# Kernel tuning notes

Hardware: AMD Instinct MI355X
Metric: run time of the kernel (lower is better)

The kernel has to match this reference:

```python
import jax, jax.numpy as jnp
import numpy as np

B, L, DM = 16, 1024, 512
DI, ST, DC, RK, OD = 1024, 16, 4, 32, 128


def setup_inputs() -> dict:
    key = jax.random.key(0)
    ks = jax.random.split(key, 10)
    s = 0.02
    x = jax.random.normal(ks[0], (B, L, DM), dtype=jnp.float32)
    W_in = jax.random.normal(ks[1], (DM, 2 * DI), dtype=jnp.float32) * s
    conv_w = jax.random.normal(ks[2], (DI, DC), dtype=jnp.float32) * 0.2
    conv_b = jax.random.normal(ks[3], (DI,), dtype=jnp.float32) * s
    W_xproj = jax.random.normal(ks[4], (DI, RK + 2 * ST), dtype=jnp.float32) * s
    W_dt = jax.random.normal(ks[5], (RK, DI), dtype=jnp.float32) * s
    b_dt = jax.random.normal(ks[6], (DI,), dtype=jnp.float32) * s
    # S4D-real init: A_log[d, n] = log(n+1)
    A_log = jnp.log(jnp.tile(jnp.arange(1, ST + 1, dtype=jnp.float32)[None, :], (DI, 1)))
    Dp = jnp.ones((DI,), dtype=jnp.float32)
    W_out = jax.random.normal(ks[7], (DI, DM), dtype=jnp.float32) * s
    W_fc = jax.random.normal(ks[8], (L * DM, OD), dtype=jnp.float32) * 0.002
    b_fc = jnp.zeros((OD,), dtype=jnp.float32)
    return {"x": x, "W_in": W_in, "conv_w": conv_w, "conv_b": conv_b,
            "W_xproj": W_xproj, "W_dt": W_dt, "b_dt": b_dt, "A_log": A_log,
            "Dp": Dp, "W_out": W_out, "W_fc": W_fc, "b_fc": b_fc}


def _silu(v):
    return v * jax.nn.sigmoid(v)


def reference(x, W_in, conv_w, conv_b, W_xproj, W_dt, b_dt, A_log, Dp, W_out, W_fc, b_fc):
    b, l, dm = x.shape
    di, dc = conv_w.shape
    rk = W_dt.shape[0]
    st = A_log.shape[1]
    # in_proj -> split into x branch and gate z
    xz = x @ W_in                                # [B,L,2*DI]
    xin, z = jnp.split(xz, 2, axis=-1)
    # causal depthwise conv1d, kernel size dc, truncated to length l
    xp = jnp.pad(xin, ((0, 0), (dc - 1, 0), (0, 0)))
    conv = conv_b
    for j in range(dc):                          # fixed small kernel loop
        conv = conv + xp[:, j:j + l, :] * conv_w[:, j]
    xc = _silu(conv)                             # [B,L,DI]
    # input-dependent dt, B, C
    x_dbl = xc @ W_xproj                         # [B,L,RK+2*ST]
    dt = jax.nn.softplus(x_dbl[..., :rk] @ W_dt + b_dt)   # [B,L,DI]
    Bm = x_dbl[..., rk:rk + st]                  # [B,L,ST]
    Cm = x_dbl[..., rk + st:]                    # [B,L,ST]
    A = -jnp.exp(A_log)                          # [DI,ST]
    # selective scan: h_t = exp(dt_t*A)*h_{t-1} + dt_t*B_t*u_t ; y_t = C_t . h_t
    def step(h, inp):
        dt_t, B_t, C_t, u_t = inp                # [B,DI],[B,ST],[B,ST],[B,DI]
        dA = jnp.exp(dt_t[:, :, None] * A)       # [B,DI,ST]
        h = h * dA + (dt_t * u_t)[:, :, None] * B_t[:, None, :]
        y = jnp.einsum('bds,bs->bd', h, C_t)
        return h, y
    h0 = jnp.zeros((b, di, st), dtype=x.dtype)
    seq = (dt.transpose(1, 0, 2), Bm.transpose(1, 0, 2),
           Cm.transpose(1, 0, 2), xc.transpose(1, 0, 2))
    _, ys = jax.lax.scan(step, h0, seq)          # ys: [L,B,DI]
    y = ys.transpose(1, 0, 2) + Dp * xc          # skip connection
    y = y * _silu(z)                             # gate
    out = y @ W_out                              # [B,L,DM]
    # flatten + fc
    return out.reshape(b, -1) @ W_fc + b_fc      # [B,OD]
```

## Files before the change

### kernel.cpp

```cpp
#include <hip/hip_runtime.h>
#include <hip/hip_bf16.h>

typedef __hip_bfloat16 bf16;
typedef __bf16 bf8v __attribute__((ext_vector_type(8)));
typedef __bf16 bf4v __attribute__((ext_vector_type(4)));
typedef float f4v __attribute__((ext_vector_type(4)));

static __device__ __forceinline__ float tf(const bf16 v) { return __bfloat162float(v); }

static __device__ __forceinline__ float ldv(const void* p, size_t i, bool f32) {
    return f32 ? ((const float*)p)[i] : tf(((const bf16*)p)[i]);
}

static __device__ __forceinline__ void gld_lds16(const bf16* g, __bf16* l) {
    __builtin_amdgcn_global_load_lds(
        (const __attribute__((address_space(1))) void*)g,
        (__attribute__((address_space(3))) void*)l, 16, 0, 0);
}

constexpr int Bz = 16, Lz = 1024, DM = 512, DI = 1024, ST = 16, DC = 4, RK = 32, OD = 128;
constexpr int Mrows = Bz * Lz;
constexpr int XD = RK + 2 * ST;
constexpr int NC = 16, CT = Lz / NC;
constexpr int FC_KC = 512;
constexpr int FC_BLOCKS = (Lz * DM) / FC_KC;

__global__ void detect_kernel(const void* __restrict__ xp, int* __restrict__ flag) {
    int i = blockIdx.x * 256 + threadIdx.x;
    const bf16* p = (const bf16*)xp;
    float v = tf(p[(size_t)i * 64]);
    if (!(fabsf(v) < 1e4f)) atomicAdd(flag, 1);
}

__global__ __launch_bounds__(256) void canon_kernel(const void* __restrict__ src,
                                                    bf16* __restrict__ dst,
                                                    const int* __restrict__ flag) {
    const bool f = (*flag != 0);
    size_t base = ((size_t)blockIdx.x * 256 + threadIdx.x) * 8;
    if (!f) {
        *(uint4*)((__bf16*)dst + base) = *(const uint4*)((const bf16*)src + base);
    } else {
        f4v a = *(const f4v*)((const float*)src + base);
        f4v b = *(const f4v*)((const float*)src + base + 4);
        bf8v o;
        #pragma unroll
        for (int j = 0; j < 4; ++j) { o[j] = (__bf16)a[j]; o[j + 4] = (__bf16)b[j]; }
        *(bf8v*)((__bf16*)dst + base) = o;
    }
}

__global__ __launch_bounds__(256) void transpose3_kernel(const void* __restrict__ W0,
                                                         const void* __restrict__ W1,
                                                         const void* __restrict__ W2,
                                                         bf16* __restrict__ T0,
                                                         bf16* __restrict__ T1,
                                                         bf16* __restrict__ T2,
                                                         const int* __restrict__ flag) {
    const bool f = (*flag != 0);
    __shared__ float tile[32][33];
    int bid = blockIdx.x;
    const void* W; bf16* Wt; int K, N, n0, k0;
    if (bid < 1024) {
        W = W0; Wt = T0; K = DM; N = 2 * DI; n0 = (bid & 63) * 32; k0 = (bid >> 6) * 32;
    } else if (bid < 1536) {
        int b = bid - 1024;
        W = W1; Wt = T1; K = DI; N = DM; n0 = (b & 15) * 32; k0 = (b >> 4) * 32;
    } else {
        int b = bid - 1536;
        W = W2; Wt = T2; K = DI; N = XD; n0 = (b & 1) * 32; k0 = (b >> 1) * 32;
    }
    int c = threadIdx.x & 31, r4 = threadIdx.x >> 5;
    #pragma unroll
    for (int i = 0; i < 4; ++i) {
        int r = r4 + i * 8;
        tile[r][c] = ldv(W, (size_t)(k0 + r) * N + n0 + c, f);
    }
    __syncthreads();
    #pragma unroll
    for (int i = 0; i < 4; ++i) {
        int rr = r4 + i * 8;
        Wt[(size_t)(n0 + rr) * K + k0 + c] = __float2bfloat16(tile[c][rr]);
    }
}

template <int NT, bool SPLIT, bool CF32, int GXL>
__global__ __launch_bounds__(256) void gemm_bt(const bf16* __restrict__ A, int lda,
                                               const bf16* __restrict__ Bt, int ldb,
                                               void* __restrict__ C0, void* __restrict__ C1,
                                               int ldc, int K) {
    constexpr int MI = (NT == 128) ? 4 : 2;
    constexpr int NI = 4;
    constexpr int GX = 1 << GXL;
    __shared__ __align__(16) __bf16 As[2][128 * 32];
    __shared__ __align__(16) __bf16 Bs[2][NT * 32];
    const int tid = threadIdx.x, lane = tid & 63, w = tid >> 6;
    const int l15 = lane & 15, quad = lane >> 4;
    const int wm = (NT == 128) ? (w >> 1) * 64 : w * 32;
    const int wn = (NT == 128) ? (w & 1) * 64 : 0;

    const int nwg = GX * gridDim.y;
    const int bid = blockIdx.y * GX + blockIdx.x;
    const int swz = (bid & 7) * (nwg >> 3) + (bid >> 3);
    const int m0 = (swz >> GXL) * 128, n0 = (swz & (GX - 1)) * NT;

    f4v acc[MI][NI];
    #pragma unroll
    for (int i = 0; i < MI; ++i)
        #pragma unroll
        for (int j = 0; j < NI; ++j)
            #pragma unroll
            for (int r = 0; r < 4; ++r) acc[i][j][r] = 0.f;

    const int arow = w * 32 + (lane >> 2), ach = lane & 3;
    const int brow = w * 16 + (lane >> 2);

    auto stage = [&](int bi, int k0) {
        {
            const bf16* g0 = A + (size_t)(m0 + arow) * lda + k0 + ach * 8;
            gld_lds16(g0, &As[bi][w * 1024 + lane * 8]);
            gld_lds16(g0 + (size_t)16 * lda, &As[bi][w * 1024 + 512 + lane * 8]);
        }
        if constexpr (NT == 128) {
            const bf16* g0 = Bt + (size_t)(n0 + arow) * ldb + k0 + ach * 8;
            gld_lds16(g0, &Bs[bi][w * 1024 + lane * 8]);
            gld_lds16(g0 + (size_t)16 * ldb, &Bs[bi][w * 1024 + 512 + lane * 8]);
        } else {
            const bf16* g0 = Bt + (size_t)(n0 + brow) * ldb + k0 + ach * 8;
            gld_lds16(g0, &Bs[bi][w * 512 + lane * 8]);
        }
    };

    stage(0, 0);
    __syncthreads();
    int cur = 0;
    for (int k0 = 0; k0 < K; k0 += 32) {
        if (k0 + 32 < K) stage(cur ^ 1, k0 + 32);
        bf8v a[MI], b[NI];
        #pragma unroll
        for (int mi = 0; mi < MI; ++mi)
            a[mi] = *(const bf8v*)&As[cur][(wm + mi * 16 + l15) * 32 + quad * 8];
        #pragma unroll
        for (int ni = 0; ni < NI; ++ni)
            b[ni] = *(const bf8v*)&Bs[cur][(wn + ni * 16 + l15) * 32 + quad * 8];
        #pragma unroll
        for (int mi = 0; mi < MI; ++mi)
            #pragma unroll
            for (int ni = 0; ni < NI; ++ni)
                acc[mi][ni] = __builtin_amdgcn_mfma_f32_16x16x32_bf16(a[mi], b[ni], acc[mi][ni], 0, 0, 0);
        __syncthreads();
        cur ^= 1;
    }
    #pragma unroll
    for (int mi = 0; mi < MI; ++mi)
        #pragma unroll
        for (int ni = 0; ni < NI; ++ni)
            #pragma unroll
            for (int r = 0; r < 4; ++r) {
                int row = m0 + wm + mi * 16 + quad * 4 + r;
                int col = n0 + wn + ni * 16 + l15;
                float v = acc[mi][ni][r];
                if (SPLIT) {
                    if (col < DI) ((bf16*)C0)[(size_t)row * DI + col] = __float2bfloat16(v);
                    else ((bf16*)C1)[(size_t)row * DI + col - DI] =
                             __float2bfloat16(v / (1.f + __expf(-v)));
                } else if (CF32) {
                    ((float*)C0)[(size_t)row * ldc + col] = v;
                } else {
                    ((bf16*)C0)[(size_t)row * ldc + col] = __float2bfloat16(v);
                }
            }
}

__global__ __launch_bounds__(256) void conv_silu_kernel(const bf16* __restrict__ xin,
                                                        const void* __restrict__ conv_w,
                                                        const void* __restrict__ conv_b,
                                                        bf16* __restrict__ xc,
                                                        const int* __restrict__ flag) {
    const bool f = (*flag != 0);
    int g = blockIdx.x * 256 + threadIdx.x;
    int d = g & (DI - 1);
    int t = (g >> 10) & (Lz - 1);
    int b = g >> 20;
    const bf16* xin_b = xin + (size_t)b * Lz * DI;
    float acc = ldv(conv_b, d, f);
    #pragma unroll
    for (int j = 0; j < DC; ++j) {
        int tt = t + j - (DC - 1);
        if (tt >= 0) acc += tf(xin_b[(size_t)tt * DI + d]) * ldv(conv_w, d * DC + j, f);
    }
    xc[(size_t)g] = __float2bfloat16(acc / (1.f + __expf(-acc)));
}

__global__ __launch_bounds__(256) void scan_pass1(const float* __restrict__ x_dbl,
                                                  const bf16* __restrict__ xc,
                                                  const void* __restrict__ A_log,
                                                  const void* __restrict__ W_dt,
                                                  const void* __restrict__ b_dt,
                                                  float* __restrict__ hbuf,
                                                  float* __restrict__ dtsum,
                                                  const int* __restrict__ flag) {
    const bool f = (*flag != 0);
    const int c = blockIdx.x, b = blockIdx.z;
    const int d = blockIdx.y * 256 + threadIdx.x;
    __shared__ float Row[CT][XD];
    #pragma unroll
    for (int i = 0; i < 4; ++i) {
        int idx = threadIdx.x + i * 256;
        int r = idx >> 4, q = idx & 15;
        *(f4v*)&Row[r][q * 4] =
            *(const f4v*)(x_dbl + ((size_t)(b * Lz + c * CT + r)) * XD + q * 4);
    }
    float W[RK];
    #pragma unroll
    for (int k = 0; k < RK; ++k) W[k] = ldv(W_dt, (size_t)k * DI + d, f);
    const float bdt = ldv(b_dt, d, f);
    float A[ST];
    #pragma unroll
    for (int s = 0; s < ST; ++s) A[s] = -__expf(ldv(A_log, (size_t)d * ST + s, f));
    __syncthreads();
    float h[ST] = {};
    float S = 0.f;
    const bf16* xcp = xc + (size_t)(b * Lz + c * CT) * DI + d;
    for (int t = 0; t < CT; ++t) {
        float acc = bdt;
        #pragma unroll
        for (int k = 0; k < RK; ++k) acc += Row[t][k] * W[k];
        float dtv = (acc > 15.f) ? acc : __logf(1.f + __expf(acc));
        float du  = dtv * tf(xcp[(size_t)t * DI]);
        S += dtv;
        #pragma unroll
        for (int s = 0; s < ST; ++s)
            h[s] = h[s] * __expf(dtv * A[s]) + du * Row[t][RK + s];
    }
    float* hp = hbuf + ((size_t)(b * DI + d) * NC + c) * 16;
    #pragma unroll
    for (int s = 0; s < ST; ++s) hp[s] = h[s];
    dtsum[(size_t)(b * DI + d) * NC + c] = S;
}

__global__ __launch_bounds__(256) void scan_prefix(float* __restrict__ hbuf,
                                                   const float* __restrict__ dtsum,
                                                   const void* __restrict__ A_log,
                                                   const int* __restrict__ flag) {
    const bool f = (*flag != 0);
    int g2 = blockIdx.x * 256 + threadIdx.x;
    int d = g2 & (DI - 1);
    float A[ST];
    #pragma unroll
    for (int s = 0; s < ST; ++s) A[s] = -__expf(ldv(A_log, (size_t)d * ST + s, f));
    float hrun[ST] = {};
    for (int c = 0; c < NC; ++c) {
        float* hp = hbuf + ((size_t)g2 * NC + c) * 16;
        float S = dtsum[(size_t)g2 * NC + c];
        #pragma unroll
        for (int s = 0; s < ST; ++s) {
            float he = hp[s];
            float P = __expf(A[s] * S);
            hp[s] = hrun[s];
            hrun[s] = hrun[s] * P + he;
        }
    }
}

__global__ __launch_bounds__(256) void scan_pass2(const float* __restrict__ x_dbl,
                                                  const bf16* __restrict__ xc,
                                                  const void* __restrict__ A_log,
                                                  const void* __restrict__ W_dt,
                                                  const void* __restrict__ b_dt,
                                                  const void* __restrict__ Dp,
                                                  bf16* __restrict__ yzs,
                                                  const float* __restrict__ hbuf,
                                                  const int* __restrict__ flag) {
    const bool f = (*flag != 0);
    const int c = blockIdx.x, b = blockIdx.z;
    const int d = blockIdx.y * 256 + threadIdx.x;
    __shared__ float Row[CT][XD];
    #pragma unroll
    for (int i = 0; i < 4; ++i) {
        int idx = threadIdx.x + i * 256;
        int r = idx >> 4, q = idx & 15;
        *(f4v*)&Row[r][q * 4] =
            *(const f4v*)(x_dbl + ((size_t)(b * Lz + c * CT + r)) * XD + q * 4);
    }
    float W[RK];
    #pragma unroll
    for (int k = 0; k < RK; ++k) W[k] = ldv(W_dt, (size_t)k * DI + d, f);
    const float bdt = ldv(b_dt, d, f);
    float A[ST];
    #pragma unroll
    for (int s = 0; s < ST; ++s) A[s] = -__expf(ldv(A_log, (size_t)d * ST + s, f));
    float Dp_d = ldv(Dp, d, f);
    __syncthreads();
    float h[ST];
    const float* hp = hbuf + ((size_t)(b * DI + d) * NC + c) * 16;
    #pragma unroll
    for (int s = 0; s < ST; ++s) h[s] = hp[s];
    const bf16* xcp = xc + (size_t)(b * Lz + c * CT) * DI + d;
    bf16*       yzp = yzs + (size_t)(b * Lz + c * CT) * DI + d;
    for (int t = 0; t < CT; ++t) {
        float acc = bdt;
        #pragma unroll
        for (int k = 0; k < RK; ++k) acc += Row[t][k] * W[k];
        float dtv = (acc > 15.f) ? acc : __logf(1.f + __expf(acc));
        float u   = tf(xcp[(size_t)t * DI]);
        float du  = dtv * u;
        float p = 0.f;
        #pragma unroll
        for (int s = 0; s < ST; ++s) {
            h[s] = h[s] * __expf(dtv * A[s]) + du * Row[t][RK + s];
            p += h[s] * Row[t][RK + ST + s];
        }
        float zz = tf(yzp[(size_t)t * DI]);
        yzp[(size_t)t * DI] = __float2bfloat16((p + Dp_d * u) * zz);
    }
}

__global__ __launch_bounds__(256) void fc_partial_kernel(const bf16* __restrict__ out_pre,
                                                         const void* __restrict__ W_fc,
                                                         float* __restrict__ part,
                                                         const int* __restrict__ flag) {
    const bool f = (*flag != 0);
    __shared__ __align__(16) float u_lds[FC_KC][16];
    const int tid = threadIdx.x;
    const int k0 = blockIdx.x * FC_KC;

    #pragma unroll
    for (int i = 0; i < 4; ++i) {
        int cid = tid + i * 256;
        int b = cid & 15, c8 = cid >> 4;
        bf8v v = *(const bf8v*)&out_pre[(size_t)b * (Lz * DM) + k0 + c8 * 8];
        #pragma unroll
        for (int j = 0; j < 8; ++j) u_lds[c8 * 8 + j][b] = (float)v[j];
    }
    __syncthreads();

    const int ng = tid & 31, kr = tid >> 5;
    f4v acc[16];
    #pragma unroll
    for (int b = 0; b < 16; ++b)
        #pragma unroll
        for (int c = 0; c < 4; ++c) acc[b][c] = 0.f;

    if (f) {
        const float* Wp = (const float*)W_fc + (size_t)(k0 + kr) * OD + ng * 4;
        #pragma unroll 4
        for (int kk = 0; kk < FC_KC; kk += 8) {
            f4v w4 = *(const f4v*)(Wp + (size_t)kk * OD);
            int kl = kk + kr;
            #pragma unroll
            for (int q = 0; q < 4; ++q) {
                f4v uq = *(const f4v*)&u_lds[kl][q * 4];
                #pragma unroll
                for (int c = 0; c < 4; ++c) acc[q * 4 + c] += uq[c] * w4;
            }
        }
    } else {
        const bf16* Wp = (const bf16*)W_fc + (size_t)(k0 + kr) * OD + ng * 4;
        #pragma unroll 4
        for (int kk = 0; kk < FC_KC; kk += 8) {
            bf4v wv = *(const bf4v*)(Wp + (size_t)kk * OD);
            f4v w4;
            #pragma unroll
            for (int c = 0; c < 4; ++c) w4[c] = (float)wv[c];
            int kl = kk + kr;
            #pragma unroll
            for (int q = 0; q < 4; ++q) {
                f4v uq = *(const f4v*)&u_lds[kl][q * 4];
                #pragma unroll
                for (int c = 0; c < 4; ++c) acc[q * 4 + c] += uq[c] * w4;
            }
        }
    }

    #pragma unroll
    for (int b = 0; b < 16; ++b)
        #pragma unroll
        for (int c = 0; c < 4; ++c) acc[b][c] += __shfl_down(acc[b][c], 32);
    __syncthreads();
    f4v* redv = (f4v*)&u_lds[0][0];
    const int w = tid >> 6, lane = tid & 63;
    if (lane < 32) {
        #pragma unroll
        for (int b = 0; b < 16; ++b) redv[(b * 4 + w) * 32 + lane] = acc[b];
    }
    __syncthreads();
    #pragma unroll
    for (int i = 0; i < 2; ++i) {
        int og = tid + i * 256;
        int b = og >> 5, ngo = og & 31;
        f4v s = {0.f, 0.f, 0.f, 0.f};
        #pragma unroll
        for (int w2 = 0; w2 < 4; ++w2) s += redv[(b * 4 + w2) * 32 + ngo];
        *(f4v*)&part[(size_t)blockIdx.x * (Bz * OD) + b * OD + ngo * 4] = s;
    }
}

__global__ __launch_bounds__(256) void fc_reduce_kernel(const float* __restrict__ part,
                                                        float* __restrict__ accb) {
    const int o = blockIdx.x * 256 + threadIdx.x;
    const int s0 = blockIdx.y * (FC_BLOCKS / 16);
    float s = 0.f;
    for (int p = s0; p < s0 + FC_BLOCKS / 16; ++p) s += part[(size_t)p * (Bz * OD) + o];
    atomicAdd(&accb[o], s);
}

__global__ void fc_final_kernel(const float* __restrict__ accbuf,
                                const void* __restrict__ b_fc, void* __restrict__ out,
                                const int* __restrict__ flag) {
    const bool f = (*flag != 0);
    int i = blockIdx.x * 256 + threadIdx.x;
    if (i < Bz * OD) {
        float v = accbuf[i] + ldv(b_fc, i & (OD - 1), f);
        if (f) ((float*)out)[i] = v;
        else   ((bf16*)out)[i]  = __float2bfloat16(v);
    }
}

extern "C" void kernel_launch(void* const* d_in, const int* in_sizes, int n_in,
                              void* d_out, int out_size, void* d_ws, size_t ws_size,
                              hipStream_t stream) {
    const void* x       = d_in[0];
    const void* W_in    = d_in[1];
    const void* conv_w  = d_in[2];
    const void* conv_b  = d_in[3];
    const void* W_xproj = d_in[4];
    const void* W_dt    = d_in[5];
    const void* b_dt    = d_in[6];
    const void* A_log   = d_in[7];
    const void* Dp      = d_in[8];
    const void* W_out   = d_in[9];
    const void* W_fc    = d_in[10];
    const void* b_fc    = d_in[11];

    char* ws = (char*)d_ws;
    bf16*     xin    = (bf16*)(ws);
    float*    part   = (float*)(ws);
    bf16*     yzs    = (bf16*)(ws + 33554432ull);
    bf16*     xc     = (bf16*)(ws + 67108864ull);
    float*    x_dbl  = (float*)(ws + 100663296ull);
    bf16*     xb     = (bf16*)(ws + 104857600ull);
    bf16*     outp   = (bf16*)(ws + 104857600ull);
    float*    hbuf   = (float*)(ws + 167772160ull);
    float*    dtsum  = (float*)(ws + 188743680ull);
    bf16*     Wt_in  = (bf16*)(ws + 199229440ull);
    bf16*     Wt_out = (bf16*)(ws + 202375168ull);
    bf16*     Wt_xp  = (bf16*)(ws + 204472320ull);
    float*    accb   = (float*)(ws + 205520896ull);
    int*      flag   = (int*)(ws + 206569472ull);

    dim3 blk(256);
    hipMemsetAsync(flag, 0, 4, stream);
    detect_kernel<<<256, blk, 0, stream>>>(x, flag);
    canon_kernel<<<(Mrows * DM) / 2048, blk, 0, stream>>>(x, xb, flag);
    transpose3_kernel<<<1600, blk, 0, stream>>>(W_in, W_out, W_xproj,
                                                Wt_in, Wt_out, Wt_xp, flag);
    hipLaunchKernelGGL((gemm_bt<128, true, false, 4>), dim3(2 * DI / 128, Mrows / 128), blk, 0, stream,
                       xb, DM, Wt_in, DM, xin, yzs, DI, DM);
    conv_silu_kernel<<<(Mrows * DI) / 256, blk, 0, stream>>>(xin, conv_w, conv_b, xc, flag);
    hipLaunchKernelGGL((gemm_bt<64, false, true, 0>), dim3(1, Mrows / 128), blk, 0, stream,
                       xc, DI, Wt_xp, DI, x_dbl, (void*)0, XD, DI);
    scan_pass1<<<dim3(NC, DI / 256, Bz), blk, 0, stream>>>(x_dbl, xc, A_log, W_dt, b_dt,
                                                           hbuf, dtsum, flag);
    scan_prefix<<<(Bz * DI) / 256, blk, 0, stream>>>(hbuf, dtsum, A_log, flag);
    scan_pass2<<<dim3(NC, DI / 256, Bz), blk, 0, stream>>>(x_dbl, xc, A_log, W_dt, b_dt,
                                                           Dp, yzs, hbuf, flag);
    hipLaunchKernelGGL((gemm_bt<128, false, false, 2>), dim3(DM / 128, Mrows / 128), blk, 0, stream,
                       yzs, DI, Wt_out, DI, outp, (void*)0, DM, DI);
    hipMemsetAsync(accb, 0, Bz * OD * sizeof(float), stream);
    fc_partial_kernel<<<FC_BLOCKS, blk, 0, stream>>>(outp, W_fc, part, flag);
    fc_reduce_kernel<<<dim3((Bz * OD) / 256, 16), blk, 0, stream>>>(part, accb);
    fc_final_kernel<<<(Bz * OD + 255) / 256, blk, 0, stream>>>(accb, b_fc, d_out, flag);
}
```

Before: 790.1 us.

## Cache dt from scan pass1, split-K x_proj GEMM, parallelize prefix over states

Scan pass1 now writes the softplus dt values as fp16 into a reused workspace region, so pass2 no longer recomputes the rank-32 dt projection and only stages the B/C columns in shared memory. The x_proj GEMM uses 64-row tiles with a 2-way split-K and atomic fp32 accumulation into a zeroed buffer, which raises block count for this skinny GEMM. The prefix kernel assigns one thread per state element instead of a 16-wide loop per thread, and the exponentials use exp2f with a pre-scaled A. Costs are an extra memset, atomics, a new dt write/read stream, and fp16 rounding of dt.

```diff
diff --git a/kernel.cpp b/kernel.cpp
--- a/kernel.cpp
+++ b/kernel.cpp
@@ -24,6 +24,7 @@
 constexpr int NC = 16, CT = Lz / NC;
 constexpr int FC_KC = 512;
 constexpr int FC_BLOCKS = (Lz * DM) / FC_KC;
+constexpr float LOG2E = 1.4426950408889634f;
 
 __global__ void detect_kernel(const void* __restrict__ xp, int* __restrict__ flag) {
     int i = blockIdx.x * 256 + threadIdx.x;
@@ -83,25 +84,25 @@
     }
 }
 
-template <int NT, bool SPLIT, bool CF32, int GXL>
+template <int MR, int NT, bool SPLIT, bool CF32, int GXL, int KS>
 __global__ __launch_bounds__(256) void gemm_bt(const bf16* __restrict__ A, int lda,
                                                const bf16* __restrict__ Bt, int ldb,
                                                void* __restrict__ C0, void* __restrict__ C1,
                                                int ldc, int K) {
-    constexpr int MI = (NT == 128) ? 4 : 2;
+    constexpr int MI = (MR == 64) ? 1 : ((NT == 128) ? 4 : 2);
     constexpr int NI = 4;
     constexpr int GX = 1 << GXL;
-    __shared__ __align__(16) __bf16 As[2][128 * 32];
+    __shared__ __align__(16) __bf16 As[2][MR * 32];
     __shared__ __align__(16) __bf16 Bs[2][NT * 32];
     const int tid = threadIdx.x, lane = tid & 63, w = tid >> 6;
     const int l15 = lane & 15, quad = lane >> 4;
-    const int wm = (NT == 128) ? (w >> 1) * 64 : w * 32;
-    const int wn = (NT == 128) ? (w & 1) * 64 : 0;
+    const int wm = (MR == 64) ? w * 16 : ((NT == 128) ? (w >> 1) * 64 : w * 32);
+    const int wn = (MR == 64) ? 0 : ((NT == 128) ? (w & 1) * 64 : 0);
 
     const int nwg = GX * gridDim.y;
     const int bid = blockIdx.y * GX + blockIdx.x;
     const int swz = (bid & 7) * (nwg >> 3) + (bid >> 3);
-    const int m0 = (swz >> GXL) * 128, n0 = (swz & (GX - 1)) * NT;
+    const int m0 = (swz >> GXL) * MR, n0 = (swz & (GX - 1)) * NT;
 
     f4v acc[MI][NI];
     #pragma unroll
@@ -111,30 +112,36 @@
             #pragma unroll
             for (int r = 0; r < 4; ++r) acc[i][j][r] = 0.f;
 
-    const int arow = w * 32 + (lane >> 2), ach = lane & 3;
-    const int brow = w * 16 + (lane >> 2);
-
     auto stage = [&](int bi, int k0) {
-        {
+        if constexpr (MR == 128) {
+            const int arow = w * 32 + (lane >> 2), ach = lane & 3;
             const bf16* g0 = A + (size_t)(m0 + arow) * lda + k0 + ach * 8;
             gld_lds16(g0, &As[bi][w * 1024 + lane * 8]);
             gld_lds16(g0 + (size_t)16 * lda, &As[bi][w * 1024 + 512 + lane * 8]);
+        } else {
+            const bf16* g0 = A + (size_t)(m0 + (tid >> 2)) * lda + k0 + (tid & 3) * 8;
+            gld_lds16(g0, &As[bi][tid * 8]);
         }
         if constexpr (NT == 128) {
+            const int arow = w * 32 + (lane >> 2), ach = lane & 3;
             const bf16* g0 = Bt + (size_t)(n0 + arow) * ldb + k0 + ach * 8;
             gld_lds16(g0, &Bs[bi][w * 1024 + lane * 8]);
             gld_lds16(g0 + (size_t)16 * ldb, &Bs[bi][w * 1024 + 512 + lane * 8]);
         } else {
-            const bf16* g0 = Bt + (size_t)(n0 + brow) * ldb + k0 + ach * 8;
-            gld_lds16(g0, &Bs[bi][w * 512 + lane * 8]);
+            const bf16* g0 = Bt + (size_t)(n0 + (tid >> 2)) * ldb + k0 + (tid & 3) * 8;
+            gld_lds16(g0, &Bs[bi][tid * 8]);
         }
     };
 
-    stage(0, 0);
+    const int kslice = K / KS;
+    const int kbeg = (KS > 1) ? (int)blockIdx.z * kslice : 0;
+    const int kend = kbeg + kslice;
+
+    stage(0, kbeg);
     __syncthreads();
     int cur = 0;
-    for (int k0 = 0; k0 < K; k0 += 32) {
-        if (k0 + 32 < K) stage(cur ^ 1, k0 + 32);
+    for (int k0 = kbeg; k0 < kend; k0 += 32) {
+        if (k0 + 32 < kend) stage(cur ^ 1, k0 + 32);
         bf8v a[MI], b[NI];
         #pragma unroll
         for (int mi = 0; mi < MI; ++mi)
@@ -164,7 +171,8 @@
                     else ((bf16*)C1)[(size_t)row * DI + col - DI] =
                              __float2bfloat16(v / (1.f + __expf(-v)));
                 } else if (CF32) {
-                    ((float*)C0)[(size_t)row * ldc + col] = v;
+                    if (KS > 1) atomicAdd(&((float*)C0)[(size_t)row * ldc + col], v);
+                    else ((float*)C0)[(size_t)row * ldc + col] = v;
                 } else {
                     ((bf16*)C0)[(size_t)row * ldc + col] = __float2bfloat16(v);
                 }
@@ -196,6 +204,7 @@
                                                   const void* __restrict__ A_log,
                                                   const void* __restrict__ W_dt,
                                                   const void* __restrict__ b_dt,
+                                                  _Float16* __restrict__ dtw,
                                                   float* __restrict__ hbuf,
                                                   float* __restrict__ dtsum,
                                                   const int* __restrict__ flag) {
@@ -214,23 +223,25 @@
     #pragma unroll
     for (int k = 0; k < RK; ++k) W[k] = ldv(W_dt, (size_t)k * DI + d, f);
     const float bdt = ldv(b_dt, d, f);
-    float A[ST];
-    #pragma unroll
-    for (int s = 0; s < ST; ++s) A[s] = -__expf(ldv(A_log, (size_t)d * ST + s, f));
+    float A2[ST];
+    #pragma unroll
+    for (int s = 0; s < ST; ++s) A2[s] = -__expf(ldv(A_log, (size_t)d * ST + s, f)) * LOG2E;
     __syncthreads();
     float h[ST] = {};
     float S = 0.f;
     const bf16* xcp = xc + (size_t)(b * Lz + c * CT) * DI + d;
+    _Float16*   dtp = dtw + (size_t)(b * Lz + c * CT) * DI + d;
     for (int t = 0; t < CT; ++t) {
         float acc = bdt;
         #pragma unroll
         for (int k = 0; k < RK; ++k) acc += Row[t][k] * W[k];
         float dtv = (acc > 15.f) ? acc : __logf(1.f + __expf(acc));
+        dtp[(size_t)t * DI] = (_Float16)dtv;
         float du  = dtv * tf(xcp[(size_t)t * DI]);
         S += dtv;
         #pragma unroll
         for (int s = 0; s < ST; ++s)
-            h[s] = h[s] * __expf(dtv * A[s]) + du * Row[t][RK + s];
+            h[s] = h[s] * exp2f(dtv * A2[s]) + du * Row[t][RK + s];
     }
     float* hp = hbuf + ((size_t)(b * DI + d) * NC + c) * 16;
     #pragma unroll
@@ -243,30 +254,24 @@
                                                    const void* __restrict__ A_log,
                                                    const int* __restrict__ flag) {
     const bool f = (*flag != 0);
-    int g2 = blockIdx.x * 256 + threadIdx.x;
+    int g = blockIdx.x * 256 + threadIdx.x;
+    int s = g & 15, g2 = g >> 4;
     int d = g2 & (DI - 1);
-    float A[ST];
-    #pragma unroll
-    for (int s = 0; s < ST; ++s) A[s] = -__expf(ldv(A_log, (size_t)d * ST + s, f));
-    float hrun[ST] = {};
+    float A2 = -__expf(ldv(A_log, (size_t)d * ST + s, f)) * LOG2E;
+    float hrun = 0.f;
     for (int c = 0; c < NC; ++c) {
-        float* hp = hbuf + ((size_t)g2 * NC + c) * 16;
+        size_t idx = ((size_t)g2 * NC + c) * 16 + s;
+        float he = hbuf[idx];
         float S = dtsum[(size_t)g2 * NC + c];
-        #pragma unroll
-        for (int s = 0; s < ST; ++s) {
-            float he = hp[s];
-            float P = __expf(A[s] * S);
-            hp[s] = hrun[s];
-            hrun[s] = hrun[s] * P + he;
-        }
+        hbuf[idx] = hrun;
+        hrun = hrun * exp2f(A2 * S) + he;
     }
 }
 
 __global__ __launch_bounds__(256) void scan_pass2(const float* __restrict__ x_dbl,
+                                                  const _Float16* __restrict__ dtw,
                                                   const bf16* __restrict__ xc,
                                                   const void* __restrict__ A_log,
-                                                  const void* __restrict__ W_dt,
-                                                  const void* __restrict__ b_dt,
                                                   const void* __restrict__ Dp,
                                                   bf16* __restrict__ yzs,
                                                   const float* __restrict__ hbuf,
@@ -274,41 +279,35 @@
     const bool f = (*flag != 0);
     const int c = blockIdx.x, b = blockIdx.z;
     const int d = blockIdx.y * 256 + threadIdx.x;
-    __shared__ float Row[CT][XD];
-    #pragma unroll
-    for (int i = 0; i < 4; ++i) {
+    __shared__ float BC[CT][32];
+    #pragma unroll
+    for (int i = 0; i < 2; ++i) {
         int idx = threadIdx.x + i * 256;
-        int r = idx >> 4, q = idx & 15;
-        *(f4v*)&Row[r][q * 4] =
-            *(const f4v*)(x_dbl + ((size_t)(b * Lz + c * CT + r)) * XD + q * 4);
-    }
-    float W[RK];
-    #pragma unroll
-    for (int k = 0; k < RK; ++k) W[k] = ldv(W_dt, (size_t)k * DI + d, f);
-    const float bdt = ldv(b_dt, d, f);
-    float A[ST];
-    #pragma unroll
-    for (int s = 0; s < ST; ++s) A[s] = -__expf(ldv(A_log, (size_t)d * ST + s, f));
+        int r = idx >> 3, q = idx & 7;
+        *(f4v*)&BC[r][q * 4] =
+            *(const f4v*)(x_dbl + ((size_t)(b * Lz + c * CT + r)) * XD + RK + q * 4);
+    }
+    float A2[ST];
+    #pragma unroll
+    for (int s = 0; s < ST; ++s) A2[s] = -__expf(ldv(A_log, (size_t)d * ST + s, f)) * LOG2E;
     float Dp_d = ldv(Dp, d, f);
     __syncthreads();
     float h[ST];
     const float* hp = hbuf + ((size_t)(b * DI + d) * NC + c) * 16;
     #pragma unroll
     for (int s = 0; s < ST; ++s) h[s] = hp[s];
-    const bf16* xcp = xc + (size_t)(b * Lz + c * CT) * DI + d;
-    bf16*       yzp = yzs + (size_t)(b * Lz + c * CT) * DI + d;
+    const _Float16* dtp = dtw + (size_t)(b * Lz + c * CT) * DI + d;
+    const bf16*     xcp = xc + (size_t)(b * Lz + c * CT) * DI + d;
+    bf16*           yzp = yzs + (size_t)(b * Lz + c * CT) * DI + d;
     for (int t = 0; t < CT; ++t) {
-        float acc = bdt;
-        #pragma unroll
-        for (int k = 0; k < RK; ++k) acc += Row[t][k] * W[k];
-        float dtv = (acc > 15.f) ? acc : __logf(1.f + __expf(acc));
+        float dtv = (float)dtp[(size_t)t * DI];
         float u   = tf(xcp[(size_t)t * DI]);
         float du  = dtv * u;
         float p = 0.f;
         #pragma unroll
         for (int s = 0; s < ST; ++s) {
-            h[s] = h[s] * __expf(dtv * A[s]) + du * Row[t][RK + s];
-            p += h[s] * Row[t][RK + ST + s];
+            h[s] = h[s] * exp2f(dtv * A2[s]) + du * BC[t][s];
+            p += h[s] * BC[t][16 + s];
         }
         float zz = tf(yzp[(size_t)t * DI]);
         yzp[(size_t)t * DI] = __float2bfloat16((p + Dp_d * u) * zz);
@@ -434,6 +433,7 @@
 
     char* ws = (char*)d_ws;
     bf16*     xin    = (bf16*)(ws);
+    _Float16* dtw    = (_Float16*)(ws);
     float*    part   = (float*)(ws);
     bf16*     yzs    = (bf16*)(ws + 33554432ull);
     bf16*     xc     = (bf16*)(ws + 67108864ull);
@@ -454,17 +454,21 @@
     canon_kernel<<<(Mrows * DM) / 2048, blk, 0, stream>>>(x, xb, flag);
     transpose3_kernel<<<1600, blk, 0, stream>>>(W_in, W_out, W_xproj,
                                                 Wt_in, Wt_out, Wt_xp, flag);
-    hipLaunchKernelGGL((gemm_bt<128, true, false, 4>), dim3(2 * DI / 128, Mrows / 128), blk, 0, stream,
+    hipLaunchKernelGGL((gemm_bt<128, 128, true, false, 4, 1>),
+                       dim3(2 * DI / 128, Mrows / 128), blk, 0, stream,
                        xb, DM, Wt_in, DM, xin, yzs, DI, DM);
     conv_silu_kernel<<<(Mrows * DI) / 256, blk, 0, stream>>>(xin, conv_w, conv_b, xc, flag);
-    hipLaunchKernelGGL((gemm_bt<64, false, true, 0>), dim3(1, Mrows / 128), blk, 0, stream,
+    hipMemsetAsync(x_dbl, 0, (size_t)Mrows * XD * sizeof(float), stream);
+    hipLaunchKernelGGL((gemm_bt<64, 64, false, true, 0, 2>),
+                       dim3(1, Mrows / 64, 2), blk, 0, stream,
                        xc, DI, Wt_xp, DI, x_dbl, (void*)0, XD, DI);
     scan_pass1<<<dim3(NC, DI / 256, Bz), blk, 0, stream>>>(x_dbl, xc, A_log, W_dt, b_dt,
-                                                           hbuf, dtsum, flag);
-    scan_prefix<<<(Bz * DI) / 256, blk, 0, stream>>>(hbuf, dtsum, A_log, flag);
-    scan_pass2<<<dim3(NC, DI / 256, Bz), blk, 0, stream>>>(x_dbl, xc, A_log, W_dt, b_dt,
+                                                           dtw, hbuf, dtsum, flag);
+    scan_prefix<<<(Bz * DI * ST) / 256, blk, 0, stream>>>(hbuf, dtsum, A_log, flag);
+    scan_pass2<<<dim3(NC, DI / 256, Bz), blk, 0, stream>>>(x_dbl, dtw, xc, A_log,
                                                            Dp, yzs, hbuf, flag);
-    hipLaunchKernelGGL((gemm_bt<128, false, false, 2>), dim3(DM / 128, Mrows / 128), blk, 0, stream,
+    hipLaunchKernelGGL((gemm_bt<128, 128, false, false, 2, 1>),
+                       dim3(DM / 128, Mrows / 128), blk, 0, stream,
                        yzs, DI, Wt_out, DI, outp, (void*)0, DM, DI);
     hipMemsetAsync(accb, 0, Bz * OD * sizeof(float), stream);
     fc_partial_kernel<<<FC_BLOCKS, blk, 0, stream>>>(outp, W_fc, part, flag);
```

Result: slower. 808.8 us (+2.4%).
